# Performance work log

Hardware: AMD Instinct MI355X
Metric: run time of the kernel (lower is better)

Reference implementation:

```python
import jax, jax.numpy as jnp
import numpy as np

T, B, W, L = 256, 128, 1024, 2


def setup_inputs() -> dict:
    key = jax.random.key(0)
    k1, k2, k3, k4 = jax.random.split(key, 4)
    scale = 1.0 / np.sqrt(W)
    return {
        "xs": jax.random.normal(k1, (T, B, W), dtype=jnp.float32),
        "resets": jax.random.bernoulli(k2, 0.05, (T, B)),
        "Wx": jax.random.normal(k3, (L, W, 4 * W), dtype=jnp.float32) * scale,
        "Wh": jax.random.normal(k4, (L, W, 4 * W), dtype=jnp.float32) * scale,
        "b": jnp.zeros((L, 4 * W), dtype=jnp.float32),
    }


def reference(xs, resets, Wx, Wh, b):
    # xs: [T,B,W], resets: [T,B] bool, Wx/Wh: [L,W,4W], b: [L,4W]
    L_, B_, W_ = Wx.shape[0], xs.shape[1], xs.shape[2]

    def step(carry, inp):
        cs, hs = carry          # each [L,B,W]
        x, r = inp              # [B,W], [B]
        m = r[None, :, None]    # reset -> reinitialize state to zeros
        cs = jnp.where(m, 0.0, cs)
        hs = jnp.where(m, 0.0, hs)
        y = x
        new_cs, new_hs = [], []
        for l in range(L_):
            z = y @ Wx[l] + hs[l] @ Wh[l] + b[l]          # [B,4W]
            i, f, g, o = jnp.split(z, 4, axis=-1)
            i = jax.nn.sigmoid(i)
            f = jax.nn.sigmoid(f)
            g = jnp.tanh(g)
            o = jax.nn.sigmoid(o)
            c = f * cs[l] + i * g
            h = o * jnp.tanh(c)
            new_cs.append(c)
            new_hs.append(h)
            y = h
        return (jnp.stack(new_cs), jnp.stack(new_hs)), y

    carry0 = (jnp.zeros((L_, B_, W_), xs.dtype), jnp.zeros((L_, B_, W_), xs.dtype))
    _, ys = jax.lax.scan(step, carry0, (xs, resets))
    return ys  # [T,B,W]
```

## Files before the change

kernel.cpp:

```cpp
#include <hip/hip_runtime.h>

#define T_   256
#define B_   128
#define W_   1024
#define G_   4096
#define NWG  256
#define NTHR 512

typedef __bf16 bf16x8 __attribute__((ext_vector_type(8)));
typedef __bf16 bf16x4 __attribute__((ext_vector_type(4)));
typedef float  f32x4  __attribute__((ext_vector_type(4)));
typedef unsigned int u32x2 __attribute__((ext_vector_type(2)));
typedef unsigned int u32x4 __attribute__((ext_vector_type(4)));

#define ZSTRIDE   18
#define LDS_Z0    131072
#define LDS_Z1    140288
#define LDS_BIAS  149504
#define LDS_TOTAL 149632

__device__ __forceinline__ float sigf(float x)   { return 1.f / (1.f + __expf(-x)); }
__device__ __forceinline__ float tanhf_(float x) { return 1.f - 2.f / (__expf(2.f * x) + 1.f); }

__device__ __forceinline__ int read_reset(const void* r, int mode, int idx) {
  if (mode == 0) return ((const int*)r)[idx] != 0;
  if (mode == 1) return ((const unsigned char*)r)[idx] != 0;
  return ((const float*)r)[idx] != 0.0f;
}

#define GLD_C(dst, p) asm volatile("global_load_dwordx4 %0, %1, off sc0 sc1" : "=v"(dst) : "v"(p))
#define GLD_N(dst, p) asm volatile("global_load_dwordx4 %0, %1, off"         : "=v"(dst) : "v"(p))
#define WAITV(N) do { asm volatile("s_waitcnt vmcnt(" #N ")" ::: "memory"); \
                      __builtin_amdgcn_sched_barrier(0); } while (0)

__device__ __forceinline__ void grid_sync(unsigned* bar, unsigned target, int wg) {
  __syncthreads();
  if (threadIdx.x == 0) {
    unsigned* sub = bar + 96 + (wg & 7) * 32;
    bool resetter = false;
    unsigned a = __hip_atomic_fetch_add(sub, 1u, __ATOMIC_RELAXED, __HIP_MEMORY_SCOPE_AGENT);
    if (a == 31) {
      unsigned ra = __hip_atomic_fetch_add(bar, 1u, __ATOMIC_RELAXED, __HIP_MEMORY_SCOPE_AGENT);
      if (ra == 7) {
        #pragma unroll
        for (int i = 0; i < 8; ++i)
          __hip_atomic_store(bar + 96 + i * 32, 0u, __ATOMIC_RELAXED, __HIP_MEMORY_SCOPE_AGENT);
        __hip_atomic_store(bar, 0u, __ATOMIC_RELAXED, __HIP_MEMORY_SCOPE_AGENT);
        asm volatile("s_waitcnt vmcnt(0)" ::: "memory");
        __hip_atomic_store(bar + 32, target, __ATOMIC_RELAXED, __HIP_MEMORY_SCOPE_AGENT);
        resetter = true;
      }
    }
    if (!resetter) {
      while (__hip_atomic_load(bar + 32, __ATOMIC_RELAXED, __HIP_MEMORY_SCOPE_AGENT) < target)
        __builtin_amdgcn_s_sleep(2);
    }
  }
  __syncthreads();
}

template <bool XBF16>
__global__ __launch_bounds__(NTHR, 2)
void lstm_scan(const float* __restrict__ xs, const void* __restrict__ rst,
               const float* __restrict__ Wx, const float* __restrict__ Wh,
               const float* __restrict__ bb, float* __restrict__ out,
               unsigned short* xsb_u, unsigned short* h0a_u, unsigned short* h0b_u,
               unsigned short* h1a_u, unsigned short* h1b_u, unsigned* bar) {
  extern __shared__ char smem[];
  __bf16* xsb = (__bf16*)xsb_u;
  __bf16* h0a = (__bf16*)h0a_u; __bf16* h0b = (__bf16*)h0b_u;
  __bf16* h1a = (__bf16*)h1a_u; __bf16* h1b = (__bf16*)h1b_u;
  const int tid = threadIdx.x;
  const int wg  = blockIdx.x;
  const int u0  = wg * 4;

  if (wg == 0) {
    const int* ri = (const int*)rst;
    unsigned f = 0;
    for (int i = tid; i < (T_ * B_) / 4; i += NTHR) {
      unsigned v = (unsigned)ri[i];
      if (v > 1u) f |= 1u;
      if (v != 0u && v != 0x3F800000u) f |= 2u;
    }
    if (f) atomicOr(bar + 64, f);
  }
  if (XBF16) {
    const int gt = wg * NTHR + tid;
    const f32x4* src = (const f32x4*)xs;
    for (int i = gt; i < (T_ * B_ * W_) / 4; i += NWG * NTHR) {
      f32x4 v = src[i];
      bf16x4 o;
      o[0] = (__bf16)v[0]; o[1] = (__bf16)v[1]; o[2] = (__bf16)v[2]; o[3] = (__bf16)v[3];
      u32x2 ov = __builtin_bit_cast(u32x2, o);
      asm volatile("global_store_dwordx2 %0, %1, off sc0 sc1" :: "v"((bf16x4*)xsb + i), "v"(ov) : "memory");
    }
  }
  {
    const int gt = wg * NTHR + tid;
    const u32x4 z4 = {0u, 0u, 0u, 0u};
    for (int i = gt; i < 65536; i += NWG * NTHR)
      asm volatile("global_store_dwordx4 %0, %1, off sc0 sc1" :: "v"((u32x4*)h0a_u + i), "v"(z4) : "memory");
  }
  {
    const int c  = tid & 15, kc = tid >> 4;
    const int col0 = ((c >> 2) << 10) + u0 + (c & 3);
    const int sw = (c & 7) << 4;
    const float* srcs[4] = { Wx, Wh, Wx + (size_t)W_ * G_, Wh + (size_t)W_ * G_ };
    for (int m = 0; m < 4; ++m) {
      const float* s = srcs[m] + col0;
      char* base = smem + m * 32768 + c * 2048;
      for (int kk = 0; kk < 32; ++kk) {
        const int k = kc * 32 + kk;
        *(__bf16*)(base + ((k * 2) ^ sw)) = (__bf16)s[(size_t)k * G_];
      }
    }
    if (tid < 32) {
      const int cc = tid & 15, l = tid >> 4;
      const int col = ((cc >> 2) << 10) + u0 + (cc & 3);
      ((float*)(smem + LDS_BIAS))[l * 16 + cc] = bb[l * G_ + col];
    }
  }
  asm volatile("s_waitcnt vmcnt(0)" ::: "memory");
  grid_sync(bar, 1u, wg);
  const unsigned mf = __hip_atomic_load(bar + 64, __ATOMIC_RELAXED, __HIP_MEMORY_SCOPE_AGENT);
  const int rmode = ((mf & 1u) == 0) ? 0 : (((mf & 2u) == 0) ? 2 : 1);

  const int lane = tid & 63, wv = tid >> 6;
  const int rq   = wv & 3;
  const int kh   = wv >> 2;
  const int lrow = lane & 15;
  const int kgrp = lane >> 4;
  const int c16  = lane & 15;
  const int swz  = (c16 & 7) << 4;
  const char* wlds = smem + c16 * 2048;
  const int row0 = (rq << 5) + lrow;
  const int row1 = row0 + 16;
  const int gb = tid >> 2, du = tid & 3;
  const int ofs = (kh << 9) + (kgrp << 3);

  float c0 = 0.f, c1 = 0.f;

  for (int p = 0; p <= T_; ++p) {
    const __bf16* h0r = (p & 1) ? h0a : h0b;
    __bf16*       h0w = (p & 1) ? h0b : h0a;
    const __bf16* h1r = (p & 1) ? h1a : h1b;
    __bf16*       h1w = (p & 1) ? h1b : h1a;
    const int tx = (p < T_) ? p : (T_ - 1);
    int r0a = (p < T_) ? read_reset(rst, rmode, p * B_ + row0) : 0;
    int r0b = (p < T_) ? read_reset(rst, rmode, p * B_ + row1) : 0;
    int r1a = (p >= 1) ? read_reset(rst, rmode, (p - 1) * B_ + row0) : 0;
    int r1b = (p >= 1) ? read_reset(rst, rmode, (p - 1) * B_ + row1) : 0;

    const __bf16* pX0  = xsb + (size_t)tx * (B_ * W_) + row0 * W_ + ofs;
    const __bf16* pX1  = xsb + (size_t)tx * (B_ * W_) + row1 * W_ + ofs;
    const float*  pXf0 = xs  + (size_t)tx * (B_ * W_) + row0 * W_ + ofs;
    const float*  pXf1 = xs  + (size_t)tx * (B_ * W_) + row1 * W_ + ofs;
    const __bf16* pH00 = h0r + row0 * W_ + ofs;
    const __bf16* pH01 = h0r + row1 * W_ + ofs;
    const __bf16* pH10 = h1r + row0 * W_ + ofs;
    const __bf16* pH11 = h1r + row1 * W_ + ofs;

    f32x4 a00 = {0.f,0.f,0.f,0.f}, a01 = {0.f,0.f,0.f,0.f};
    f32x4 a10 = {0.f,0.f,0.f,0.f}, a11 = {0.f,0.f,0.f,0.f};
    const bf16x8 z8 = {};

    asm volatile("" :: "v"(r0a), "v"(r0b), "v"(r1a), "v"(r1b));
    asm volatile("s_waitcnt vmcnt(0)" ::: "memory");

    if constexpr (XBF16) {
      f32x4 Px0,Px1,P00,P01,P10,P11, Qx0,Qx1,Q00,Q01,Q10,Q11;
      GLD_N(Px0, pX0);  GLD_N(Px1, pX1);
      GLD_C(P00, pH00); GLD_C(P01, pH01); GLD_C(P10, pH10); GLD_C(P11, pH11);

#define KSTEP_B(CX0,CX1,C00,C01,C10,C11, NX0,NX1,N00,N01,N10,N11, KI, ISNEXT) \
      { \
        if (ISNEXT) { \
          const int no = ((KI) + 1) * 32; \
          GLD_N(NX0, pX0 + no);  GLD_N(NX1, pX1 + no); \
          GLD_C(N00, pH00 + no); GLD_C(N01, pH01 + no); \
          GLD_C(N10, pH10 + no); GLD_C(N11, pH11 + no); \
        } \
        const int koff = ((kh << 10) + ((KI) << 6) + (kgrp << 4)) ^ swz; \
        bf16x8 w0 = *(const bf16x8*)(wlds +     0 + koff); \
        bf16x8 w1 = *(const bf16x8*)(wlds + 32768 + koff); \
        bf16x8 w2 = *(const bf16x8*)(wlds + 65536 + koff); \
        bf16x8 w3 = *(const bf16x8*)(wlds + 98304 + koff); \
        if (ISNEXT) { WAITV(6); } else { WAITV(0); } \
        bf16x8 ax0 = __builtin_bit_cast(bf16x8, CX0); \
        bf16x8 ax1 = __builtin_bit_cast(bf16x8, CX1); \
        bf16x8 b00 = __builtin_bit_cast(bf16x8, C00); \
        bf16x8 b01 = __builtin_bit_cast(bf16x8, C01); \
        bf16x8 b10 = __builtin_bit_cast(bf16x8, C10); \
        bf16x8 b11 = __builtin_bit_cast(bf16x8, C11); \
        a00 = __builtin_amdgcn_mfma_f32_16x16x32_bf16(ax0, w0, a00, 0, 0, 0); \
        a00 = __builtin_amdgcn_mfma_f32_16x16x32_bf16(r0a ? z8 : b00, w1, a00, 0, 0, 0); \
        a10 = __builtin_amdgcn_mfma_f32_16x16x32_bf16(b00, w2, a10, 0, 0, 0); \
        a10 = __builtin_amdgcn_mfma_f32_16x16x32_bf16(r1a ? z8 : b10, w3, a10, 0, 0, 0); \
        a01 = __builtin_amdgcn_mfma_f32_16x16x32_bf16(ax1, w0, a01, 0, 0, 0); \
        a01 = __builtin_amdgcn_mfma_f32_16x16x32_bf16(r0b ? z8 : b01, w1, a01, 0, 0, 0); \
        a11 = __builtin_amdgcn_mfma_f32_16x16x32_bf16(b01, w2, a11, 0, 0, 0); \
        a11 = __builtin_amdgcn_mfma_f32_16x16x32_bf16(r1b ? z8 : b11, w3, a11, 0, 0, 0); \
      }

      #pragma unroll
      for (int kp = 0; kp < 8; ++kp) {
        KSTEP_B(Px0,Px1,P00,P01,P10,P11, Qx0,Qx1,Q00,Q01,Q10,Q11, 2*kp,   1);
        KSTEP_B(Qx0,Qx1,Q00,Q01,Q10,Q11, Px0,Px1,P00,P01,P10,P11, 2*kp+1, (kp < 7));
      }
#undef KSTEP_B
    } else {
      f32x4 Pxa0,Pxb0,Pxa1,Pxb1,P00,P01,P10,P11, Qxa0,Qxb0,Qxa1,Qxb1,Q00,Q01,Q10,Q11;
      GLD_N(Pxa0, pXf0); GLD_N(Pxb0, pXf0 + 4);
      GLD_N(Pxa1, pXf1); GLD_N(Pxb1, pXf1 + 4);
      GLD_C(P00, pH00);  GLD_C(P01, pH01); GLD_C(P10, pH10); GLD_C(P11, pH11);

#define KSTEP_F(CXA0,CXB0,CXA1,CXB1,C00,C01,C10,C11, NXA0,NXB0,NXA1,NXB1,N00,N01,N10,N11, KI, ISNEXT) \
      { \
        if (ISNEXT) { \
          const int no = ((KI) + 1) * 32; \
          GLD_N(NXA0, pXf0 + no); GLD_N(NXB0, pXf0 + no + 4); \
          GLD_N(NXA1, pXf1 + no); GLD_N(NXB1, pXf1 + no + 4); \
          GLD_C(N00, pH00 + no);  GLD_C(N01, pH01 + no); \
          GLD_C(N10, pH10 + no);  GLD_C(N11, pH11 + no); \
        } \
        const int koff = ((kh << 10) + ((KI) << 6) + (kgrp << 4)) ^ swz; \
        bf16x8 w0 = *(const bf16x8*)(wlds +     0 + koff); \
        bf16x8 w1 = *(const bf16x8*)(wlds + 32768 + koff); \
        bf16x8 w2 = *(const bf16x8*)(wlds + 65536 + koff); \
        bf16x8 w3 = *(const bf16x8*)(wlds + 98304 + koff); \
        if (ISNEXT) { WAITV(8); } else { WAITV(0); } \
        bf16x8 ax0, ax1; \
        _Pragma("unroll") \
        for (int j = 0; j < 4; ++j) { \
          ax0[j] = (__bf16)CXA0[j]; ax0[4+j] = (__bf16)CXB0[j]; \
          ax1[j] = (__bf16)CXA1[j]; ax1[4+j] = (__bf16)CXB1[j]; \
        } \
        bf16x8 b00 = __builtin_bit_cast(bf16x8, C00); \
        bf16x8 b01 = __builtin_bit_cast(bf16x8, C01); \
        bf16x8 b10 = __builtin_bit_cast(bf16x8, C10); \
        bf16x8 b11 = __builtin_bit_cast(bf16x8, C11); \
        a00 = __builtin_amdgcn_mfma_f32_16x16x32_bf16(ax0, w0, a00, 0, 0, 0); \
        a00 = __builtin_amdgcn_mfma_f32_16x16x32_bf16(r0a ? z8 : b00, w1, a00, 0, 0, 0); \
        a10 = __builtin_amdgcn_mfma_f32_16x16x32_bf16(b00, w2, a10, 0, 0, 0); \
        a10 = __builtin_amdgcn_mfma_f32_16x16x32_bf16(r1a ? z8 : b10, w3, a10, 0, 0, 0); \
        a01 = __builtin_amdgcn_mfma_f32_16x16x32_bf16(ax1, w0, a01, 0, 0, 0); \
        a01 = __builtin_amdgcn_mfma_f32_16x16x32_bf16(r0b ? z8 : b01, w1, a01, 0, 0, 0); \
        a11 = __builtin_amdgcn_mfma_f32_16x16x32_bf16(b01, w2, a11, 0, 0, 0); \
        a11 = __builtin_amdgcn_mfma_f32_16x16x32_bf16(r1b ? z8 : b11, w3, a11, 0, 0, 0); \
      }

      #pragma unroll
      for (int kp = 0; kp < 8; ++kp) {
        KSTEP_F(Pxa0,Pxb0,Pxa1,Pxb1,P00,P01,P10,P11, Qxa0,Qxb0,Qxa1,Qxb1,Q00,Q01,Q10,Q11, 2*kp,   1);
        KSTEP_F(Qxa0,Qxb0,Qxa1,Qxb1,Q00,Q01,Q10,Q11, Pxa0,Pxb0,Pxa1,Pxb1,P00,P01,P10,P11, 2*kp+1, (kp < 7));
      }
#undef KSTEP_F
    }

    {
      float* z0 = (float*)(smem + LDS_Z0);
      float* z1 = (float*)(smem + LDS_Z1);
      const int zr0 = (rq << 5) + (kgrp << 2);
      const int zr1 = zr0 + 16;
      if (kh == 0) {
        if (p < T_) {
          #pragma unroll
          for (int v = 0; v < 4; ++v) { z0[(zr0+v)*ZSTRIDE + c16] = a00[v]; z0[(zr1+v)*ZSTRIDE + c16] = a01[v]; }
        }
        if (p >= 1) {
          #pragma unroll
          for (int v = 0; v < 4; ++v) { z1[(zr0+v)*ZSTRIDE + c16] = a10[v]; z1[(zr1+v)*ZSTRIDE + c16] = a11[v]; }
        }
      }
      __syncthreads();
      if (kh == 1) {
        if (p < T_) {
          #pragma unroll
          for (int v = 0; v < 4; ++v) { z0[(zr0+v)*ZSTRIDE + c16] += a00[v]; z0[(zr1+v)*ZSTRIDE + c16] += a01[v]; }
        }
        if (p >= 1) {
          #pragma unroll
          for (int v = 0; v < 4; ++v) { z1[(zr0+v)*ZSTRIDE + c16] += a10[v]; z1[(zr1+v)*ZSTRIDE + c16] += a11[v]; }
        }
      }
      __syncthreads();
    }

    const float* bz = (const float*)(smem + LDS_BIAS);
    if (p < T_) {
      const float* z0 = (const float*)(smem + LDS_Z0);
      const float zi = z0[gb * ZSTRIDE + du]      + bz[du];
      const float zf = z0[gb * ZSTRIDE + 4 + du]  + bz[4 + du];
      const float zg = z0[gb * ZSTRIDE + 8 + du]  + bz[8 + du];
      const float zo = z0[gb * ZSTRIDE + 12 + du] + bz[12 + du];
      const float ii = sigf(zi), ff = sigf(zf), gg = tanhf_(zg), oo = sigf(zo);
      if (read_reset(rst, rmode, p * B_ + gb)) c0 = 0.f;
      c0 = ff * c0 + ii * gg;
      const float h = oo * tanhf_(c0);
      unsigned hv = (unsigned)__builtin_bit_cast(unsigned short, (__bf16)h);
      asm volatile("global_store_short %0, %1, off sc0 sc1" :: "v"(h0w + gb * W_ + u0 + du), "v"(hv) : "memory");
    }
    if (p >= 1) {
      const float* z1 = (const float*)(smem + LDS_Z1);
      const float zi = z1[gb * ZSTRIDE + du]      + bz[16 + du];
      const float zf = z1[gb * ZSTRIDE + 4 + du]  + bz[20 + du];
      const float zg = z1[gb * ZSTRIDE + 8 + du]  + bz[24 + du];
      const float zo = z1[gb * ZSTRIDE + 12 + du] + bz[28 + du];
      const float ii = sigf(zi), ff = sigf(zf), gg = tanhf_(zg), oo = sigf(zo);
      if (read_reset(rst, rmode, (p - 1) * B_ + gb)) c1 = 0.f;
      c1 = ff * c1 + ii * gg;
      const float h = oo * tanhf_(c1);
      unsigned hv = (unsigned)__builtin_bit_cast(unsigned short, (__bf16)h);
      asm volatile("global_store_short %0, %1, off sc0 sc1" :: "v"(h1w + gb * W_ + u0 + du), "v"(hv) : "memory");
      out[(size_t)(p - 1) * (B_ * W_) + gb * W_ + u0 + du] = h;
    }
    asm volatile("s_waitcnt vmcnt(0)" ::: "memory");
    grid_sync(bar, (unsigned)(p + 2), wg);
  }
}

extern "C" void kernel_launch(void* const* d_in, const int* in_sizes, int n_in,
                              void* d_out, int out_size, void* d_ws, size_t ws_size,
                              hipStream_t stream) {
  const float* xs  = (const float*)d_in[0];
  const void*  rst = (const void*)d_in[1];
  const float* Wx  = (const float*)d_in[2];
  const float* Wh  = (const float*)d_in[3];
  const float* bb  = (const float*)d_in[4];
  float* out = (float*)d_out;

  char* ws = (char*)d_ws;
  const size_t xsb_bytes = (size_t)T_ * B_ * W_ * 2;
  const size_t h_bytes   = (size_t)4 * B_ * W_ * 2;
  const bool xb = ws_size >= xsb_bytes + h_bytes + 2048;

  unsigned short* xsb = (unsigned short*)ws;
  char* hbase = xb ? (ws + xsb_bytes) : ws;
  unsigned short* h0a = (unsigned short*)hbase;
  unsigned short* h0b = h0a + B_ * W_;
  unsigned short* h1a = h0b + B_ * W_;
  unsigned short* h1b = h1a + B_ * W_;
  unsigned* bar = (unsigned*)(hbase + h_bytes);

  hipMemsetAsync(bar, 0, 2048, stream);

  void* args[] = { (void*)&xs, (void*)&rst, (void*)&Wx, (void*)&Wh, (void*)&bb, (void*)&out,
                   (void*)&xsb, (void*)&h0a, (void*)&h0b, (void*)&h1a, (void*)&h1b, (void*)&bar };

  if (xb) {
    (void)hipFuncSetAttribute(reinterpret_cast<const void*>(&lstm_scan<true>),
                              hipFuncAttributeMaxDynamicSharedMemorySize, LDS_TOTAL);
    (void)hipLaunchCooperativeKernel(reinterpret_cast<const void*>(&lstm_scan<true>),
                                     dim3(NWG), dim3(NTHR), args, LDS_TOTAL, stream);
  } else {
    (void)hipFuncSetAttribute(reinterpret_cast<const void*>(&lstm_scan<false>),
                              hipFuncAttributeMaxDynamicSharedMemorySize, LDS_TOTAL);
    (void)hipLaunchCooperativeKernel(reinterpret_cast<const void*>(&lstm_scan<false>),
                                     dim3(NWG), dim3(NTHR), args, LDS_TOTAL, stream);
  }
}
```

Baseline: 7.013 ms.

## Use multi-slot hidden-state ring buffers to allow cached loads of h

After: 7.208 ms. 2.8% more time.

```diff
diff --git a/kernel.cpp b/kernel.cpp
--- a/kernel.cpp
+++ b/kernel.cpp
@@ -6,6 +6,9 @@
 #define G_   4096
 #define NWG  256
 #define NTHR 512
+#define SLE  131072
+#define NSLOT 258
+#define SSTRIDE 127
 
 typedef __bf16 bf16x8 __attribute__((ext_vector_type(8)));
 typedef __bf16 bf16x4 __attribute__((ext_vector_type(4)));
@@ -30,6 +33,7 @@
 
 #define GLD_C(dst, p) asm volatile("global_load_dwordx4 %0, %1, off sc0 sc1" : "=v"(dst) : "v"(p))
 #define GLD_N(dst, p) asm volatile("global_load_dwordx4 %0, %1, off"         : "=v"(dst) : "v"(p))
+#define GLD_H(dst, p) do { if constexpr (MODE == 0 || MODE == 3) { GLD_N(dst, p); } else { GLD_C(dst, p); } } while (0)
 #define WAITV(N) do { asm volatile("s_waitcnt vmcnt(" #N ")" ::: "memory"); \
                       __builtin_amdgcn_sched_barrier(0); } while (0)
 
@@ -59,17 +63,17 @@
   __syncthreads();
 }
 
-template <bool XBF16>
+template <int MODE>
 __global__ __launch_bounds__(NTHR, 2)
 void lstm_scan(const float* __restrict__ xs, const void* __restrict__ rst,
                const float* __restrict__ Wx, const float* __restrict__ Wh,
                const float* __restrict__ bb, float* __restrict__ out,
-               unsigned short* xsb_u, unsigned short* h0a_u, unsigned short* h0b_u,
-               unsigned short* h1a_u, unsigned short* h1b_u, unsigned* bar) {
+               unsigned short* xsb_u, unsigned short* r0_u, unsigned short* r1_u,
+               unsigned* bar) {
   extern __shared__ char smem[];
   __bf16* xsb = (__bf16*)xsb_u;
-  __bf16* h0a = (__bf16*)h0a_u; __bf16* h0b = (__bf16*)h0b_u;
-  __bf16* h1a = (__bf16*)h1a_u; __bf16* h1b = (__bf16*)h1b_u;
+  __bf16* ring0 = (__bf16*)r0_u;
+  __bf16* ring1 = (__bf16*)r1_u;
   const int tid = threadIdx.x;
   const int wg  = blockIdx.x;
   const int u0  = wg * 4;
@@ -84,7 +88,7 @@
     }
     if (f) atomicOr(bar + 64, f);
   }
-  if (XBF16) {
+  if (MODE == 0 || MODE == 1) {
     const int gt = wg * NTHR + tid;
     const f32x4* src = (const f32x4*)xs;
     for (int i = gt; i < (T_ * B_ * W_) / 4; i += NWG * NTHR) {
@@ -98,8 +102,15 @@
   {
     const int gt = wg * NTHR + tid;
     const u32x4 z4 = {0u, 0u, 0u, 0u};
-    for (int i = gt; i < 65536; i += NWG * NTHR)
-      asm volatile("global_store_dwordx4 %0, %1, off sc0 sc1" :: "v"((u32x4*)h0a_u + i), "v"(z4) : "memory");
+    if constexpr (MODE == 0 || MODE == 3) {
+      for (int i = gt; i < SLE / 8; i += NWG * NTHR) {
+        asm volatile("global_store_dwordx4 %0, %1, off sc0 sc1" :: "v"((u32x4*)r0_u + i), "v"(z4) : "memory");
+        asm volatile("global_store_dwordx4 %0, %1, off sc0 sc1" :: "v"((u32x4*)r1_u + i), "v"(z4) : "memory");
+      }
+    } else {
+      for (int i = gt; i < 65536; i += NWG * NTHR)
+        asm volatile("global_store_dwordx4 %0, %1, off sc0 sc1" :: "v"((u32x4*)r0_u + i), "v"(z4) : "memory");
+    }
   }
   {
     const int c  = tid & 15, kc = tid >> 4;
@@ -139,12 +150,14 @@
   const int ofs = (kh << 9) + (kgrp << 3);
 
   float c0 = 0.f, c1 = 0.f;
+  int slot_r = 0, slot_w = SSTRIDE;
 
   for (int p = 0; p <= T_; ++p) {
-    const __bf16* h0r = (p & 1) ? h0a : h0b;
-    __bf16*       h0w = (p & 1) ? h0b : h0a;
-    const __bf16* h1r = (p & 1) ? h1a : h1b;
-    __bf16*       h1w = (p & 1) ? h1b : h1a;
+    if constexpr (MODE == 1 || MODE == 2) { slot_r = (p + 1) & 1; slot_w = p & 1; }
+    const __bf16* h0r = ring0 + (size_t)slot_r * SLE;
+    __bf16*       h0w = ring0 + (size_t)slot_w * SLE;
+    const __bf16* h1r = ring1 + (size_t)slot_r * SLE;
+    __bf16*       h1w = ring1 + (size_t)slot_w * SLE;
     const int tx = (p < T_) ? p : (T_ - 1);
     int r0a = (p < T_) ? read_reset(rst, rmode, p * B_ + row0) : 0;
     int r0b = (p < T_) ? read_reset(rst, rmode, p * B_ + row1) : 0;
@@ -167,18 +180,18 @@
     asm volatile("" :: "v"(r0a), "v"(r0b), "v"(r1a), "v"(r1b));
     asm volatile("s_waitcnt vmcnt(0)" ::: "memory");
 
-    if constexpr (XBF16) {
+    if constexpr (MODE == 0 || MODE == 1) {
       f32x4 Px0,Px1,P00,P01,P10,P11, Qx0,Qx1,Q00,Q01,Q10,Q11;
       GLD_N(Px0, pX0);  GLD_N(Px1, pX1);
-      GLD_C(P00, pH00); GLD_C(P01, pH01); GLD_C(P10, pH10); GLD_C(P11, pH11);
+      GLD_H(P00, pH00); GLD_H(P01, pH01); GLD_H(P10, pH10); GLD_H(P11, pH11);
 
 #define KSTEP_B(CX0,CX1,C00,C01,C10,C11, NX0,NX1,N00,N01,N10,N11, KI, ISNEXT) \
       { \
         if (ISNEXT) { \
           const int no = ((KI) + 1) * 32; \
           GLD_N(NX0, pX0 + no);  GLD_N(NX1, pX1 + no); \
-          GLD_C(N00, pH00 + no); GLD_C(N01, pH01 + no); \
-          GLD_C(N10, pH10 + no); GLD_C(N11, pH11 + no); \
+          GLD_H(N00, pH00 + no); GLD_H(N01, pH01 + no); \
+          GLD_H(N10, pH10 + no); GLD_H(N11, pH11 + no); \
         } \
         const int koff = ((kh << 10) + ((KI) << 6) + (kgrp << 4)) ^ swz; \
         bf16x8 w0 = *(const bf16x8*)(wlds +     0 + koff); \
@@ -212,7 +225,7 @@
       f32x4 Pxa0,Pxb0,Pxa1,Pxb1,P00,P01,P10,P11, Qxa0,Qxb0,Qxa1,Qxb1,Q00,Q01,Q10,Q11;
       GLD_N(Pxa0, pXf0); GLD_N(Pxb0, pXf0 + 4);
       GLD_N(Pxa1, pXf1); GLD_N(Pxb1, pXf1 + 4);
-      GLD_C(P00, pH00);  GLD_C(P01, pH01); GLD_C(P10, pH10); GLD_C(P11, pH11);
+      GLD_H(P00, pH00);  GLD_H(P01, pH01); GLD_H(P10, pH10); GLD_H(P11, pH11);
 
 #define KSTEP_F(CXA0,CXB0,CXA1,CXB1,C00,C01,C10,C11, NXA0,NXB0,NXA1,NXB1,N00,N01,N10,N11, KI, ISNEXT) \
       { \
@@ -220,8 +233,8 @@
           const int no = ((KI) + 1) * 32; \
           GLD_N(NXA0, pXf0 + no); GLD_N(NXB0, pXf0 + no + 4); \
           GLD_N(NXA1, pXf1 + no); GLD_N(NXB1, pXf1 + no + 4); \
-          GLD_C(N00, pH00 + no);  GLD_C(N01, pH01 + no); \
-          GLD_C(N10, pH10 + no);  GLD_C(N11, pH11 + no); \
+          GLD_H(N00, pH00 + no);  GLD_H(N01, pH01 + no); \
+          GLD_H(N10, pH10 + no);  GLD_H(N11, pH11 + no); \
         } \
         const int koff = ((kh << 10) + ((KI) << 6) + (kgrp << 4)) ^ swz; \
         bf16x8 w0 = *(const bf16x8*)(wlds +     0 + koff); \
@@ -314,6 +327,10 @@
       asm volatile("global_store_short %0, %1, off sc0 sc1" :: "v"(h1w + gb * W_ + u0 + du), "v"(hv) : "memory");
       out[(size_t)(p - 1) * (B_ * W_) + gb * W_ + u0 + du] = h;
     }
+    if constexpr (MODE == 0 || MODE == 3) {
+      slot_r = slot_w;
+      slot_w += SSTRIDE; if (slot_w >= NSLOT) slot_w -= NSLOT;
+    }
     asm volatile("s_waitcnt vmcnt(0)" ::: "memory");
     grid_sync(bar, (unsigned)(p + 2), wg);
   }
@@ -330,32 +347,62 @@
   float* out = (float*)d_out;
 
   char* ws = (char*)d_ws;
+  const size_t slb       = (size_t)SLE * 2;
   const size_t xsb_bytes = (size_t)T_ * B_ * W_ * 2;
-  const size_t h_bytes   = (size_t)4 * B_ * W_ * 2;
-  const bool xb = ws_size >= xsb_bytes + h_bytes + 2048;
-
-  unsigned short* xsb = (unsigned short*)ws;
-  char* hbase = xb ? (ws + xsb_bytes) : ws;
-  unsigned short* h0a = (unsigned short*)hbase;
-  unsigned short* h0b = h0a + B_ * W_;
-  unsigned short* h1a = h0b + B_ * W_;
-  unsigned short* h1b = h1a + B_ * W_;
-  unsigned* bar = (unsigned*)(hbase + h_bytes);
-
-  hipMemsetAsync(bar, 0, 2048, stream);
+  const size_t ring_bytes = 2 * (size_t)NSLOT * slb;
+  const size_t need0 = 4096 + xsb_bytes + ring_bytes;
+  const size_t need3 = 4096 + ring_bytes;
+  const size_t need1 = 4096 + xsb_bytes + 4 * slb;
+
+  unsigned* bar = (unsigned*)ws;
+  (void)hipMemsetAsync(bar, 0, 4096, stream);
+
+  unsigned short *xsb, *r0, *r1;
+  int mode;
+  if (ws_size >= need0) {
+    mode = 0;
+    xsb = (unsigned short*)(ws + 4096);
+    r0  = (unsigned short*)(ws + 4096 + xsb_bytes);
+    r1  = r0 + (size_t)NSLOT * SLE;
+  } else if (ws_size >= need3) {
+    mode = 3;
+    xsb = (unsigned short*)(ws + 4096);
+    r0  = (unsigned short*)(ws + 4096);
+    r1  = r0 + (size_t)NSLOT * SLE;
+  } else if (ws_size >= need1) {
+    mode = 1;
+    xsb = (unsigned short*)(ws + 4096);
+    r0  = (unsigned short*)(ws + 4096 + xsb_bytes);
+    r1  = r0 + 2 * SLE;
+  } else {
+    mode = 2;
+    xsb = (unsigned short*)(ws + 4096);
+    r0  = (unsigned short*)(ws + 4096);
+    r1  = r0 + 2 * SLE;
+  }
 
   void* args[] = { (void*)&xs, (void*)&rst, (void*)&Wx, (void*)&Wh, (void*)&bb, (void*)&out,
-                   (void*)&xsb, (void*)&h0a, (void*)&h0b, (void*)&h1a, (void*)&h1b, (void*)&bar };
-
-  if (xb) {
-    (void)hipFuncSetAttribute(reinterpret_cast<const void*>(&lstm_scan<true>),
+                   (void*)&xsb, (void*)&r0, (void*)&r1, (void*)&bar };
+
+  if (mode == 0) {
+    (void)hipFuncSetAttribute(reinterpret_cast<const void*>(&lstm_scan<0>),
                               hipFuncAttributeMaxDynamicSharedMemorySize, LDS_TOTAL);
-    (void)hipLaunchCooperativeKernel(reinterpret_cast<const void*>(&lstm_scan<true>),
+    (void)hipLaunchCooperativeKernel(reinterpret_cast<const void*>(&lstm_scan<0>),
+                                     dim3(NWG), dim3(NTHR), args, LDS_TOTAL, stream);
+  } else if (mode == 3) {
+    (void)hipFuncSetAttribute(reinterpret_cast<const void*>(&lstm_scan<3>),
+                              hipFuncAttributeMaxDynamicSharedMemorySize, LDS_TOTAL);
+    (void)hipLaunchCooperativeKernel(reinterpret_cast<const void*>(&lstm_scan<3>),
+                                     dim3(NWG), dim3(NTHR), args, LDS_TOTAL, stream);
+  } else if (mode == 1) {
+    (void)hipFuncSetAttribute(reinterpret_cast<const void*>(&lstm_scan<1>),
+                              hipFuncAttributeMaxDynamicSharedMemorySize, LDS_TOTAL);
+    (void)hipLaunchCooperativeKernel(reinterpret_cast<const void*>(&lstm_scan<1>),
                                      dim3(NWG), dim3(NTHR), args, LDS_TOTAL, stream);
   } else {
-    (void)hipFuncSetAttribute(reinterpret_cast<const void*>(&lstm_scan<false>),
+    (void)hipFuncSetAttribute(reinterpret_cast<const void*>(&lstm_scan<2>),
                               hipFuncAttributeMaxDynamicSharedMemorySize, LDS_TOTAL);
-    (void)hipLaunchCooperativeKernel(reinterpret_cast<const void*>(&lstm_scan<false>),
+    (void)hipLaunchCooperativeKernel(reinterpret_cast<const void*>(&lstm_scan<2>),
                                      dim3(NWG), dim3(NTHR), args, LDS_TOTAL, stream);
   }
 }
```
